# Kernel tuning notes

Hardware: AMD Instinct MI355X
Metric: run time of the kernel (lower is better)

The kernel has to match this reference:

```python
import jax, jax.numpy as jnp
import numpy as np

K = 20        # kNN neighborhood size (args.k)
EPS = 1e-5    # BatchNorm eps
SLOPE = 0.2   # LeakyReLU negative slope
B, N = 8, 2048


def lrelu(x):
    return jnp.where(x >= 0, x, SLOPE * x)


def bn_cn(x):  # BatchNorm1d over [B, C, N] (training-mode batch stats, gamma=1, beta=0)
    m = jnp.mean(x, axis=(0, 2), keepdims=True)
    v = jnp.var(x, axis=(0, 2), keepdims=True)
    return (x - m) * jax.lax.rsqrt(v + EPS)


def bn_f(x):  # BatchNorm1d over [B, F]
    m = jnp.mean(x, axis=0, keepdims=True)
    v = jnp.var(x, axis=0, keepdims=True)
    return (x - m) * jax.lax.rsqrt(v + EPS)


def conv_bn(x, w):  # 1x1 Conv1d (no bias) + BN + LeakyReLU; x [B,C,N], w [O,C]
    return lrelu(bn_cn(jnp.einsum('oc,bcn->bon', w, x)))


def knn_idx(x, k):  # x [B,C,N] -> [B,N,k] nearest neighbors, self excluded
    sq = jnp.sum(x * x, axis=1)                                   # [B,N]
    pd = 2.0 * jnp.einsum('bcn,bcm->bnm', x, x) - sq[:, :, None] - sq[:, None, :]
    return jax.lax.top_k(pd, k + 1)[1][:, :, 1:]                  # drop self (max = 0)


def self_att(x, wq, wk, wv, wc):  # SelfAttention block (n_heads=1, scale_dot)
    idx = knn_idx(x, K)                                           # [B,N,K]
    feats = jnp.swapaxes(x, 1, 2)                                 # [B,N,C]
    nb = jax.vmap(lambda f, i: f[i])(feats, idx)                  # [B,N,K,C] gather
    E = wq.shape[0]
    q = feats @ wq.T                                              # [B,N,E]
    kk = nb @ wk.T                                                # [B,N,K,E]
    v = (nb - feats[:, :, None, :]) @ wv.T                        # [B,N,K,V]
    scores = jax.nn.softmax(jnp.einsum('bne,bnke->bnk', q, kk) / np.float32(np.sqrt(E)), axis=-1)
    out = jnp.einsum('bnk,bnkv->bnv', scores, v)                  # [B,N,V]
    res = conv_bn(jnp.swapaxes(out, 1, 2), wc)                    # [B,O,N]
    return jnp.concatenate([res, x], axis=1)


def setup_inputs() -> dict:
    key = jax.random.key(0)
    ks = jax.random.split(key, 32)
    w = lambda k, o, i: jax.random.normal(k, (o, i), jnp.float32) / np.float32(np.sqrt(i))
    d = {'x': jax.random.normal(ks[0], (B, 3, N), jnp.float32)}
    dims = {1: 3, 2: 64, 3: 64, 4: 128}
    j = 1
    for s, c in dims.items():
        for nm in ('wq', 'wk', 'wv', 'wc'):
            d[f'sa{s}_{nm}'] = w(ks[j], c, c); j += 1
    d['conv1_w'] = w(ks[17], 64, 6)
    d['conv2_w'] = w(ks[18], 64, 128)
    d['conv3_w'] = w(ks[19], 128, 128)
    d['conv4_w'] = w(ks[20], 256, 256)
    d['conv5_w'] = w(ks[21], 1024, 512)
    d['lin1_w'] = w(ks[22], 512, 2048); d['lin1_b'] = jnp.zeros((512,), jnp.float32)
    d['lin2_w'] = w(ks[23], 256, 512);  d['lin2_b'] = jnp.zeros((256,), jnp.float32)
    d['lin3_w'] = w(ks[24], 40, 256);   d['lin3_b'] = jnp.zeros((40,), jnp.float32)
    return d


def reference(x, sa1_wq, sa1_wk, sa1_wv, sa1_wc, sa2_wq, sa2_wk, sa2_wv, sa2_wc,
              sa3_wq, sa3_wk, sa3_wv, sa3_wc, sa4_wq, sa4_wk, sa4_wv, sa4_wc,
              conv1_w, conv2_w, conv3_w, conv4_w, conv5_w,
              lin1_w, lin1_b, lin2_w, lin2_b, lin3_w, lin3_b):
    h = self_att(x, sa1_wq, sa1_wk, sa1_wv, sa1_wc)        # [B,6,N]
    x1 = conv_bn(h, conv1_w)                               # [B,64,N]
    h = self_att(x1, sa2_wq, sa2_wk, sa2_wv, sa2_wc)       # [B,128,N]
    x2 = conv_bn(h, conv2_w)                               # [B,64,N]
    h = self_att(x2, sa3_wq, sa3_wk, sa3_wv, sa3_wc)       # [B,128,N]
    x3 = conv_bn(h, conv3_w)                               # [B,128,N]
    h = self_att(x3, sa4_wq, sa4_wk, sa4_wv, sa4_wc)       # [B,256,N]
    x4 = conv_bn(h, conv4_w)                               # [B,256,N]
    xc = jnp.concatenate([x1, x2, x3, x4], axis=1)         # [B,512,N]
    x5 = conv_bn(xc, conv5_w)                              # [B,1024,N]
    p = jnp.concatenate([jnp.max(x5, axis=2), jnp.mean(x5, axis=2)], axis=1)  # [B,2048]
    h = lrelu(bn_f(p @ lin1_w.T + lin1_b))                 # dropout = identity (eval)
    h = lrelu(bn_f(h @ lin2_w.T + lin2_b))
    return h @ lin3_w.T + lin3_b                           # [B,40]
```

## Files before the change

kernel.cpp:

```cpp
#include <hip/hip_runtime.h>
#include <math.h>

#define BB 8
#define NN 2048
#define KNB 20

typedef __attribute__((ext_vector_type(8))) short bf16x8;
typedef __attribute__((ext_vector_type(8))) _Float16 f16x8;
typedef __attribute__((ext_vector_type(4))) float f32x4;

__device__ inline unsigned short f2bf(float f) {
  union { float f; unsigned u; } v; v.f = f;
  unsigned r = v.u + 0x7FFF + ((v.u >> 16) & 1);
  return (unsigned short)(r >> 16);
}

__device__ inline float lrelu(float v) { return v >= 0.f ? v : 0.2f * v; }

template <bool F16SPLIT, bool BF16>
__global__ __launch_bounds__(256) void xprep_kernel(
    const float* __restrict__ in, int inBS, int C,
    float* __restrict__ xT, _Float16* __restrict__ hi, _Float16* __restrict__ lo,
    unsigned short* __restrict__ bf, float* __restrict__ sq) {
  __shared__ float tile[32][33];
  __shared__ float ps[8][33];
  int b = blockIdx.z;
  const float* ip = in + (size_t)b * inBS;
  int c0 = blockIdx.x * 32;
  int r0 = blockIdx.y * 32;
  int tx = threadIdx.x & 31, ty = threadIdx.x >> 5;
  float s = 0.f;
  for (int yy = ty; yy < 32; yy += 8) {
    int r = r0 + yy;
    float v = (r < C) ? ip[(size_t)r * NN + c0 + tx] : 0.f;
    tile[yy][tx] = v;
    s += v * v;
  }
  ps[ty][tx] = s;
  __syncthreads();
  if (ty == 0) {
    float a = ps[0][tx];
#pragma unroll
    for (int u = 1; u < 8; ++u) a += ps[u][tx];
    atomicAdd(&sq[b * NN + c0 + tx], a);
  }
  for (int yy = ty; yy < 32; yy += 8) {
    int c = c0 + yy, r = r0 + tx;
    if (r < C) {
      float v = tile[tx][yy];
      size_t o = (size_t)b * NN * C + (size_t)c * C + r;
      xT[o] = v;
      if (F16SPLIT) {
        _Float16 hv = (_Float16)v;
        hi[o] = hv;
        lo[o] = (_Float16)(v - (float)hv);
      }
      if (BF16) bf[o] = f2bf(v);
    }
  }
}

__global__ __launch_bounds__(256) void xprep3_kernel(const float* __restrict__ in,
                                                     float* __restrict__ xT,
                                                     float* __restrict__ xs4) {
  int b = blockIdx.z;
  int n = blockIdx.x * 256 + threadIdx.x;
  const float* ip = in + (size_t)b * 3 * NN;
  float x0 = ip[n], x1 = ip[NN + n], x2 = ip[2 * NN + n];
  float s = x0 * x0 + x1 * x1 + x2 * x2;
  size_t o = (size_t)b * NN + n;
  xT[o * 3 + 0] = x0; xT[o * 3 + 1] = x1; xT[o * 3 + 2] = x2;
  *(float4*)&xs4[o * 4] = make_float4(x0, x1, x2, s);
}

__global__ __launch_bounds__(256) void prep_mw_kernel(
    const float* __restrict__ wq, const float* __restrict__ wk,
    const float* __restrict__ wv, const float* __restrict__ wc, int C,
    float* __restrict__ M, float* __restrict__ WCV,
    unsigned short* __restrict__ Mb, unsigned short* __restrict__ wcvb, int emitBF) {
  int w = blockIdx.x * 4 + (threadIdx.x >> 6);
  int lane = threadIdx.x & 63;
  int total = 2 * C * C;
  if (w >= total) return;
  float a = 0.f;
  if (w < C * C) {
    int c = w / C, cp = w - c * C;
    for (int e = lane; e < C; e += 64) a += wk[e * C + c] * wq[e * C + cp];
  } else {
    int t = w - C * C;
    int o = t / C, c = t - o * C;
    for (int e = lane; e < C; e += 64) a += wc[o * C + e] * wv[e * C + c];
  }
#pragma unroll
  for (int s = 32; s > 0; s >>= 1) a += __shfl_down(a, s);
  if (lane == 0) {
    if (w < C * C) {
      M[w] = a;
      if (emitBF) Mb[w] = f2bf(a);
    } else {
      int t = w - C * C;
      WCV[t] = a;
      if (emitBF) wcvb[t] = f2bf(a);
    }
  }
}

__global__ __launch_bounds__(256) void convert_bf16_kernel(const float* __restrict__ in,
                                                           unsigned short* __restrict__ out,
                                                           int count) {
  int i = blockIdx.x * 256 + threadIdx.x;
  if (i < count) out[i] = f2bf(in[i]);
}

__global__ __launch_bounds__(256) void transpose_kernel(const float* __restrict__ in, int inBS,
                                                        int R, int Cl, float* __restrict__ out) {
  __shared__ float tile[32][33];
  int b = blockIdx.z;
  const float* ip = in + (size_t)b * inBS;
  float* op = out + (size_t)b * R * Cl;
  int c0 = blockIdx.x * 32, r0 = blockIdx.y * 32;
  int tx = threadIdx.x & 31, ty = threadIdx.x >> 5;
  for (int yy = ty; yy < 32; yy += 8) {
    int r = r0 + yy, c = c0 + tx;
    tile[yy][tx] = (r < R && c < Cl) ? ip[(size_t)r * Cl + c] : 0.f;
  }
  __syncthreads();
  for (int yy = ty; yy < 32; yy += 8) {
    int c = c0 + yy, r = r0 + tx;
    if (c < Cl && r < R) op[(size_t)c * R + r] = tile[tx][yy];
  }
}

__global__ __launch_bounds__(256) void transpose_bf16_kernel(const float* __restrict__ in, int inBS,
                                                             int R, int Cl,
                                                             unsigned short* __restrict__ out) {
  __shared__ float tile[32][33];
  int b = blockIdx.z;
  const float* ip = in + (size_t)b * inBS;
  unsigned short* op = out + (size_t)b * R * Cl;
  int c0 = blockIdx.x * 32, r0 = blockIdx.y * 32;
  int tx = threadIdx.x & 31, ty = threadIdx.x >> 5;
  for (int yy = ty; yy < 32; yy += 8) {
    int r = r0 + yy, c = c0 + tx;
    tile[yy][tx] = (r < R && c < Cl) ? ip[(size_t)r * Cl + c] : 0.f;
  }
  __syncthreads();
  for (int yy = ty; yy < 32; yy += 8) {
    int c = c0 + yy, r = r0 + tx;
    if (c < Cl && r < R) op[(size_t)c * R + r] = f2bf(tile[tx][yy]);
  }
}

__global__ __launch_bounds__(256, 2) void mfma_gemm_lds_kernel(
    const unsigned short* __restrict__ A, const unsigned short* __restrict__ B,
    float* __restrict__ Z, int O, int K) {
  const int b = blockIdx.z;
  const int n0 = blockIdx.x * 128, o0 = blockIdx.y * 128;
  const int tid = threadIdx.x;
  const int wave = tid >> 6, lane = tid & 63;
  const int wo = wave >> 1, wn = wave & 1;
  const int l16 = lane & 15, q = lane >> 4;
  __shared__ unsigned short Al[2][4096];
  __shared__ unsigned short Bl[2][4096];
  const unsigned short* Ab = A + (size_t)o0 * K;
  const unsigned short* Bb = B + ((size_t)b * NN + n0) * K;

  const int p0 = tid, p1 = tid + 256;
  const int r0 = ((p0 >> 6) << 4) | (p0 & 15), c0 = ((p0 >> 4) & 3) * 8;
  const int r1 = ((p1 >> 6) << 4) | (p1 & 15), c1 = ((p1 >> 4) & 3) * 8;

  bf16x8 ar0, ar1, br0, br1;
  auto gload = [&](int k0) {
    ar0 = *(const bf16x8*)(Ab + (size_t)r0 * K + k0 + c0);
    ar1 = *(const bf16x8*)(Ab + (size_t)r1 * K + k0 + c1);
    br0 = *(const bf16x8*)(Bb + (size_t)r0 * K + k0 + c0);
    br1 = *(const bf16x8*)(Bb + (size_t)r1 * K + k0 + c1);
  };
  auto sstore = [&](int buf) {
    *(bf16x8*)&Al[buf][p0 * 8] = ar0;
    *(bf16x8*)&Al[buf][p1 * 8] = ar1;
    *(bf16x8*)&Bl[buf][p0 * 8] = br0;
    *(bf16x8*)&Bl[buf][p1 * 8] = br1;
  };

  f32x4 acc[4][4];
#pragma unroll
  for (int s = 0; s < 4; ++s)
#pragma unroll
    for (int t = 0; t < 4; ++t) acc[s][t] = (f32x4){0.f, 0.f, 0.f, 0.f};

  gload(0);
  sstore(0);
  int cur = 0;
  for (int k0 = 0; k0 < K; k0 += 32) {
    bool more = (k0 + 32) < K;
    if (more) gload(k0 + 32);
    __syncthreads();
    bf16x8 af[4], bfr[4];
#pragma unroll
    for (int s = 0; s < 4; ++s)
      af[s] = *(const bf16x8*)&Al[cur][((wo * 4 + s) * 64 + q * 16 + l16) * 8];
#pragma unroll
    for (int t = 0; t < 4; ++t)
      bfr[t] = *(const bf16x8*)&Bl[cur][((wn * 4 + t) * 64 + q * 16 + l16) * 8];
#pragma unroll
    for (int s = 0; s < 4; ++s)
#pragma unroll
      for (int t = 0; t < 4; ++t)
        acc[s][t] = __builtin_amdgcn_mfma_f32_16x16x32_bf16(af[s], bfr[t], acc[s][t], 0, 0, 0);
    if (more) sstore(cur ^ 1);
    cur ^= 1;
  }
#pragma unroll
  for (int s = 0; s < 4; ++s)
#pragma unroll
    for (int t = 0; t < 4; ++t) {
      float* zp = Z + ((size_t)b * O + o0 + wo * 64 + s * 16 + q * 4) * NN
                  + n0 + wn * 64 + t * 16 + l16;
#pragma unroll
      for (int r = 0; r < 4; ++r) zp[(size_t)r * NN] = acc[s][t][r];
    }
}

__global__ __launch_bounds__(256, 2) void pd_mfma_kernel(
    const _Float16* __restrict__ xhi, const _Float16* __restrict__ xlo, int C,
    const float* __restrict__ sq, float* __restrict__ P, int b_base) {
  const int bl = blockIdx.z;
  const int b = b_base + bl;
  const int n0 = blockIdx.x * 128, m0 = blockIdx.y * 128;
  const int tid = threadIdx.x;
  const int wave = tid >> 6, lane = tid & 63;
  const int wn_ = wave >> 1, wm_ = wave & 1;
  const int l16 = lane & 15, q = lane >> 4;
  __shared__ _Float16 Ah[4096], Al[4096], Bh[4096], Bl[4096];
  const _Float16* Ahg = xhi + ((size_t)b * NN + n0) * C;
  const _Float16* Alg = xlo + ((size_t)b * NN + n0) * C;
  const _Float16* Bhg = xhi + ((size_t)b * NN + m0) * C;
  const _Float16* Blg = xlo + ((size_t)b * NN + m0) * C;

  const int p0 = tid, p1 = tid + 256;
  const int r0 = ((p0 >> 6) << 4) | (p0 & 15), c0 = ((p0 >> 4) & 3) * 8;
  const int r1 = ((p1 >> 6) << 4) | (p1 & 15), c1 = ((p1 >> 4) & 3) * 8;

  f32x4 acc[4][4];
#pragma unroll
  for (int s = 0; s < 4; ++s)
#pragma unroll
    for (int t = 0; t < 4; ++t) acc[s][t] = (f32x4){0.f, 0.f, 0.f, 0.f};

  for (int k0 = 0; k0 < C; k0 += 32) {
    __syncthreads();
    *(f16x8*)&Ah[p0 * 8] = *(const f16x8*)(Ahg + (size_t)r0 * C + k0 + c0);
    *(f16x8*)&Ah[p1 * 8] = *(const f16x8*)(Ahg + (size_t)r1 * C + k0 + c1);
    *(f16x8*)&Al[p0 * 8] = *(const f16x8*)(Alg + (size_t)r0 * C + k0 + c0);
    *(f16x8*)&Al[p1 * 8] = *(const f16x8*)(Alg + (size_t)r1 * C + k0 + c1);
    *(f16x8*)&Bh[p0 * 8] = *(const f16x8*)(Bhg + (size_t)r0 * C + k0 + c0);
    *(f16x8*)&Bh[p1 * 8] = *(const f16x8*)(Bhg + (size_t)r1 * C + k0 + c1);
    *(f16x8*)&Bl[p0 * 8] = *(const f16x8*)(Blg + (size_t)r0 * C + k0 + c0);
    *(f16x8*)&Bl[p1 * 8] = *(const f16x8*)(Blg + (size_t)r1 * C + k0 + c1);
    __syncthreads();
    f16x8 ah[4], al[4], bh[4], blv[4];
#pragma unroll
    for (int s = 0; s < 4; ++s) {
      int pi = ((wn_ * 4 + s) * 64 + q * 16 + l16) * 8;
      ah[s] = *(const f16x8*)&Ah[pi];
      al[s] = *(const f16x8*)&Al[pi];
    }
#pragma unroll
    for (int t = 0; t < 4; ++t) {
      int pi = ((wm_ * 4 + t) * 64 + q * 16 + l16) * 8;
      bh[t] = *(const f16x8*)&Bh[pi];
      blv[t] = *(const f16x8*)&Bl[pi];
    }
#pragma unroll
    for (int s = 0; s < 4; ++s)
#pragma unroll
      for (int t = 0; t < 4; ++t) {
        acc[s][t] = __builtin_amdgcn_mfma_f32_16x16x32_f16(ah[s], bh[t], acc[s][t], 0, 0, 0);
        acc[s][t] = __builtin_amdgcn_mfma_f32_16x16x32_f16(ah[s], blv[t], acc[s][t], 0, 0, 0);
        acc[s][t] = __builtin_amdgcn_mfma_f32_16x16x32_f16(al[s], bh[t], acc[s][t], 0, 0, 0);
      }
  }
#pragma unroll
  for (int s = 0; s < 4; ++s)
#pragma unroll
    for (int t = 0; t < 4; ++t) {
      int col = m0 + wm_ * 64 + t * 16 + l16;
      float sqv = sq[b * NN + col];
      float* pp = P + ((size_t)bl * NN + n0 + wn_ * 64 + s * 16 + q * 4) * NN + col;
#pragma unroll
      for (int r = 0; r < 4; ++r) pp[(size_t)r * NN] = 2.f * acc[s][t][r] - sqv;
    }
}

__global__ __launch_bounds__(256) void topk_bsort_kernel(const float* __restrict__ P,
                                                         int* __restrict__ idx_out, int b_base) {
  const int wave = threadIdx.x >> 6;
  const int lane = threadIdx.x & 63;
  const int n = blockIdx.x * 4 + wave;
  const int bl = blockIdx.y;
  const int b = b_base + bl;
  const float4* rp = (const float4*)(P + ((size_t)bl * NN + n) * NN);
  unsigned key[32];
#pragma unroll
  for (int q = 0; q < 8; ++q) {
    float4 vv = rp[q * 64 + lane];
    int mb = q * 256 + lane * 4;
    float fv[4] = {vv.x, vv.y, vv.z, vv.w};
#pragma unroll
    for (int j = 0; j < 4; ++j) {
      unsigned u = __float_as_uint(fv[j]);
      unsigned mask = (unsigned)(((int)u) >> 31) | 0x80000000u;
      unsigned sl = (unsigned)(q * 4 + j);
      key[q * 4 + j] = (mb + j == n) ? sl : (((u ^ mask) & 0xFFFFFFE0u) | sl);
    }
  }
#pragma unroll
  for (int k = 2; k <= 32; k <<= 1) {
#pragma unroll
    for (int j = k >> 1; j > 0; j >>= 1) {
#pragma unroll
      for (int i = 0; i < 32; ++i) {
        int l = i ^ j;
        if (l > i) {
          unsigned ka = key[i], kb = key[l];
          unsigned mx = ka > kb ? ka : kb;
          unsigned mn = ka > kb ? kb : ka;
          if ((i & k) == 0) { key[i] = mx; key[l] = mn; }
          else              { key[i] = mn; key[l] = mx; }
        }
      }
    }
  }
  int* op = idx_out + (size_t)(b * NN + n) * KNB;
  for (int k = 0; k < KNB; ++k) {
    unsigned best = key[0];
#pragma unroll
    for (int s = 32; s > 0; s >>= 1) {
      unsigned o = (unsigned)__shfl_xor((int)best, s);
      best = best > o ? best : o;
    }
    unsigned long long bal = __ballot(key[0] == best);
    if (lane == (int)__ffsll(bal) - 1) {
      unsigned sl = key[0] & 31u;
      op[k] = (int)((sl >> 2) * 256u + (unsigned)lane * 4u + (sl & 3u));
#pragma unroll
      for (int j = 0; j < 20; ++j) key[j] = key[j + 1];
    }
  }
}

__global__ __launch_bounds__(256) void topk_c3_kernel(const float* __restrict__ xs4,
                                                      int* __restrict__ idx_out) {
  const int wave = threadIdx.x >> 6;
  const int lane = threadIdx.x & 63;
  const int n = blockIdx.x * 4 + wave;
  const int b = blockIdx.y;
  const float4* xp = (const float4*)(xs4 + (size_t)b * NN * 4);
  float4 me = xp[n];
  float tx = 2.f * me.x, ty = 2.f * me.y, tz = 2.f * me.z;
  unsigned key[32];
#pragma unroll
  for (int s = 0; s < 32; ++s) {
    int m = s * 64 + lane;
    float4 c = xp[m];
    float pd = tx * c.x + ty * c.y + tz * c.z - c.w;
    unsigned u = __float_as_uint(pd);
    unsigned mask = (unsigned)(((int)u) >> 31) | 0x80000000u;
    key[s] = (m == n) ? (unsigned)s : ((((u ^ mask) & 0xFFFFFFE0u)) | (unsigned)s);
  }
#pragma unroll
  for (int k = 2; k <= 32; k <<= 1) {
#pragma unroll
    for (int j = k >> 1; j > 0; j >>= 1) {
#pragma unroll
      for (int i = 0; i < 32; ++i) {
        int l = i ^ j;
        if (l > i) {
          unsigned ka = key[i], kb = key[l];
          unsigned mx = ka > kb ? ka : kb;
          unsigned mn = ka > kb ? kb : ka;
          if ((i & k) == 0) { key[i] = mx; key[l] = mn; }
          else              { key[i] = mn; key[l] = mx; }
        }
      }
    }
  }
  int* op = idx_out + (size_t)(b * NN + n) * KNB;
  for (int k = 0; k < KNB; ++k) {
    unsigned best = key[0];
#pragma unroll
    for (int s = 32; s > 0; s >>= 1) {
      unsigned o = (unsigned)__shfl_xor((int)best, s);
      best = best > o ? best : o;
    }
    unsigned long long bal = __ballot(key[0] == best);
    if (lane == (int)__ffsll(bal) - 1) {
      unsigned sl = key[0] & 31u;
      op[k] = (int)(sl * 64u + (unsigned)lane);
#pragma unroll
      for (int j = 0; j < 20; ++j) key[j] = key[j + 1];
    }
  }
}

__global__ __launch_bounds__(256, 2) void conv_gemm_kernel(
    const float* __restrict__ in, int inBS, int C, int O,
    const float* __restrict__ w, float* __restrict__ z) {
  const int b = blockIdx.z;
  const int n0 = blockIdx.x * 64, o0 = blockIdx.y * 64;
  const int tid = threadIdx.x;
  const int tm = tid & 15, tn = tid >> 4;
  __shared__ float Ws[16][68];
  __shared__ float Xs[16][64];
  const float* ib = in + (size_t)b * inBS;
  float acc[4][4];
#pragma unroll
  for (int i = 0; i < 4; ++i)
#pragma unroll
    for (int j = 0; j < 4; ++j) acc[i][j] = 0.f;

  for (int k0 = 0; k0 < C; k0 += 16) {
    __syncthreads();
#pragma unroll
    for (int it = 0; it < 4; ++it) {
      int i = it * 256 + tid;
      int kc = i >> 6, nl = i & 63;
      Xs[kc][nl] = ((k0 + kc) < C) ? ib[(size_t)(k0 + kc) * NN + n0 + nl] : 0.f;
      int ol = i >> 4, kc2 = i & 15;
      Ws[kc2][ol] = ((o0 + ol) < O && (k0 + kc2) < C) ? w[(size_t)(o0 + ol) * C + k0 + kc2] : 0.f;
    }
    __syncthreads();
#pragma unroll
    for (int kc = 0; kc < 16; ++kc) {
      float4 a = *(const float4*)&Ws[kc][tn * 4];
      float4 bv = *(const float4*)&Xs[kc][tm * 4];
      acc[0][0] += a.x * bv.x; acc[0][1] += a.x * bv.y; acc[0][2] += a.x * bv.z; acc[0][3] += a.x * bv.w;
      acc[1][0] += a.y * bv.x; acc[1][1] += a.y * bv.y; acc[1][2] += a.y * bv.z; acc[1][3] += a.y * bv.w;
      acc[2][0] += a.z * bv.x; acc[2][1] += a.z * bv.y; acc[2][2] += a.z * bv.z; acc[2][3] += a.z * bv.w;
      acc[3][0] += a.w * bv.x; acc[3][1] += a.w * bv.y; acc[3][2] += a.w * bv.z; acc[3][3] += a.w * bv.w;
    }
  }
#pragma unroll
  for (int i = 0; i < 4; ++i) {
    int o = o0 + tn * 4 + i;
    if (o < O) {
      float4 ov;
      ov.x = acc[i][0]; ov.y = acc[i][1]; ov.z = acc[i][2]; ov.w = acc[i][3];
      *(float4*)&z[((size_t)b * O + o) * NN + n0 + tm * 4] = ov;
    }
  }
}

__global__ __launch_bounds__(256, 2) void conv_gemm128_db_kernel(
    const float* __restrict__ in, int inBS, int C, int O,
    const float* __restrict__ w, float* __restrict__ z) {
  const int b = blockIdx.z;
  const int n0 = blockIdx.x * 128, o0 = blockIdx.y * 128;
  const int tid = threadIdx.x;
  const int tm = tid & 15, tn = tid >> 4;
  __shared__ float Xs[2][16][128];
  __shared__ float Ws[2][16][132];
  const float* ib = in + (size_t)b * inBS;
  float acc[8][8];
#pragma unroll
  for (int i = 0; i < 8; ++i)
#pragma unroll
    for (int j = 0; j < 8; ++j) acc[i][j] = 0.f;

  float4 xr[2], wr[2];
  auto load_tile = [&](int k0) {
#pragma unroll
    for (int it = 0; it < 2; ++it) {
      int i = it * 256 + tid;
      int kc = i >> 5, c4 = i & 31;
      xr[it] = ((k0 + kc) < C) ? *(const float4*)&ib[(size_t)(k0 + kc) * NN + n0 + c4 * 4]
                               : make_float4(0.f, 0.f, 0.f, 0.f);
      int ol = i >> 2, kq = i & 3;
      wr[it] = ((k0 + kq * 4) < C) ? *(const float4*)&w[(size_t)(o0 + ol) * C + k0 + kq * 4]
                                   : make_float4(0.f, 0.f, 0.f, 0.f);
    }
  };
  auto store_tile = [&](int buf) {
#pragma unroll
    for (int it = 0; it < 2; ++it) {
      int i = it * 256 + tid;
      int kc = i >> 5, c4 = i & 31;
      *(float4*)&Xs[buf][kc][c4 * 4] = xr[it];
      int ol = i >> 2, kq = i & 3;
      Ws[buf][kq * 4 + 0][ol] = wr[it].x;
      Ws[buf][kq * 4 + 1][ol] = wr[it].y;
      Ws[buf][kq * 4 + 2][ol] = wr[it].z;
      Ws[buf][kq * 4 + 3][ol] = wr[it].w;
    }
  };

  load_tile(0);
  store_tile(0);
  int cur = 0;
  for (int k0 = 0; k0 < C; k0 += 16) {
    bool more = (k0 + 16) < C;
    if (more) load_tile(k0 + 16);
    __syncthreads();
#pragma unroll
    for (int kc = 0; kc < 16; ++kc) {
      float4 a0 = *(const float4*)&Ws[cur][kc][tn * 4];
      float4 a1 = *(const float4*)&Ws[cur][kc][64 + tn * 4];
      float4 b0 = *(const float4*)&Xs[cur][kc][tm * 4];
      float4 b1 = *(const float4*)&Xs[cur][kc][64 + tm * 4];
      float ar[8] = {a0.x, a0.y, a0.z, a0.w, a1.x, a1.y, a1.z, a1.w};
      float br[8] = {b0.x, b0.y, b0.z, b0.w, b1.x, b1.y, b1.z, b1.w};
#pragma unroll
      for (int i = 0; i < 8; ++i)
#pragma unroll
        for (int j = 0; j < 8; ++j) acc[i][j] += ar[i] * br[j];
    }
    if (more) store_tile(cur ^ 1);
    cur ^= 1;
  }
#pragma unroll
  for (int h = 0; h < 2; ++h)
#pragma unroll
    for (int i = 0; i < 4; ++i) {
      int r = h * 4 + i;
      int o = o0 + h * 64 + tn * 4 + i;
      float* zrow = &z[((size_t)b * O + o) * NN + n0];
      float4 o0v, o1v;
      o0v.x = acc[r][0]; o0v.y = acc[r][1]; o0v.z = acc[r][2]; o0v.w = acc[r][3];
      o1v.x = acc[r][4]; o1v.y = acc[r][5]; o1v.z = acc[r][6]; o1v.w = acc[r][7];
      *(float4*)&zrow[tm * 4] = o0v;
      *(float4*)&zrow[64 + tm * 4] = o1v;
    }
}

template <int C, bool BF16OUT>
__global__ __launch_bounds__(64) void att_wave_kernel(
    const float* __restrict__ xT, const float* __restrict__ UT,
    const int* __restrict__ idx, float* __restrict__ AGGt,
    unsigned short* __restrict__ AGGtb) {
  const int n = blockIdx.x & (NN - 1);
  const int b = blockIdx.x >> 11;
  const int lane = threadIdx.x;
  constexpr int CP = C + 1;
  __shared__ float nb[KNB][CP];
  __shared__ float sl[KNB];
  __shared__ int nidx[KNB];
  __shared__ float ul[C];
  const float* xTb = xT + (size_t)b * NN * C;
  if (lane < KNB) nidx[lane] = idx[(size_t)(b * NN + n) * KNB + lane];
  for (int c = lane; c < C; c += 64) ul[c] = UT[((size_t)b * NN + n) * C + c];
  __syncthreads();
  for (int i = lane; i < KNB * C; i += 64) {
    int k = i / C, c = i - k * C;
    nb[k][c] = xTb[(size_t)nidx[k] * C + c];
  }
  __syncthreads();
  float sv = -INFINITY;
  if (lane < KNB) {
    float a = 0.f;
#pragma unroll
    for (int c = 0; c < C; ++c) a += nb[lane][c] * ul[c];
    sv = a / sqrtf((float)C);
  }
  float mx = sv;
#pragma unroll
  for (int s = 32; s > 0; s >>= 1) mx = fmaxf(mx, __shfl_xor(mx, s));
  float e = (lane < KNB) ? expf(sv - mx) : 0.f;
  float sum = e;
#pragma unroll
  for (int s = 32; s > 0; s >>= 1) sum += __shfl_xor(sum, s);
  if (lane < KNB) sl[lane] = e / sum;
  __syncthreads();
  const float* xTn = xTb + (size_t)n * C;
  for (int c = lane; c < C; c += 64) {
    float a = 0.f;
#pragma unroll
    for (int k = 0; k < KNB; ++k) a += sl[k] * nb[k][c];
    float r = a - xTn[c];
    if (BF16OUT)
      AGGtb[((size_t)b * NN + n) * C + c] = f2bf(r);
    else
      AGGt[((size_t)b * NN + n) * C + c] = r;
  }
}

__global__ __launch_bounds__(256) void bn_fused_kernel(const float* __restrict__ z, int O,
                                                       float* __restrict__ out, int outBS, int c0) {
  int o = blockIdx.x;
  int tid = threadIdx.x;
  __shared__ float s1[256], s2[256];
  __shared__ float smv, srv;
  float a1 = 0.f, a2 = 0.f;
  for (int i = tid; i < BB * 512; i += 256) {
    int b = i >> 9, n4 = i & 511;
    float4 v = *(const float4*)&z[((size_t)b * O + o) * NN + n4 * 4];
    a1 += v.x + v.y + v.z + v.w;
    a2 += v.x * v.x + v.y * v.y + v.z * v.z + v.w * v.w;
  }
  s1[tid] = a1; s2[tid] = a2;
  __syncthreads();
  for (int st = 128; st > 0; st >>= 1) {
    if (tid < st) { s1[tid] += s1[tid + st]; s2[tid] += s2[tid + st]; }
    __syncthreads();
  }
  if (tid == 0) {
    float m = s1[0] / (BB * NN);
    float var = s2[0] / (BB * NN) - m * m;
    smv = m; srv = rsqrtf(var + 1e-5f);
  }
  __syncthreads();
  float m = smv, r = srv;
  for (int i = tid; i < BB * 512; i += 256) {
    int b = i >> 9, n4 = i & 511;
    float4 v = *(const float4*)&z[((size_t)b * O + o) * NN + n4 * 4];
    float4 ov;
    ov.x = lrelu((v.x - m) * r); ov.y = lrelu((v.y - m) * r);
    ov.z = lrelu((v.z - m) * r); ov.w = lrelu((v.w - m) * r);
    *(float4*)&out[(size_t)b * outBS + (size_t)(c0 + o) * NN + n4 * 4] = ov;
  }
}

__global__ __launch_bounds__(256) void bn_copy_kernel(const float* __restrict__ z, int O,
                                                      const float* __restrict__ xin, int xbs,
                                                      float* __restrict__ out) {
  int o = blockIdx.x;
  int tid = threadIdx.x;
  int outBS = 2 * O * NN;
  if (o >= O) {
    int c = o - O;
    for (int i = tid; i < BB * 512; i += 256) {
      int b = i >> 9, n4 = i & 511;
      *(float4*)&out[(size_t)b * outBS + (size_t)o * NN + n4 * 4] =
          *(const float4*)&xin[(size_t)b * xbs + (size_t)c * NN + n4 * 4];
    }
    return;
  }
  __shared__ float s1[256], s2[256];
  __shared__ float smv, srv;
  float a1 = 0.f, a2 = 0.f;
  for (int i = tid; i < BB * 512; i += 256) {
    int b = i >> 9, n4 = i & 511;
    float4 v = *(const float4*)&z[((size_t)b * O + o) * NN + n4 * 4];
    a1 += v.x + v.y + v.z + v.w;
    a2 += v.x * v.x + v.y * v.y + v.z * v.z + v.w * v.w;
  }
  s1[tid] = a1; s2[tid] = a2;
  __syncthreads();
  for (int st = 128; st > 0; st >>= 1) {
    if (tid < st) { s1[tid] += s1[tid + st]; s2[tid] += s2[tid + st]; }
    __syncthreads();
  }
  if (tid == 0) {
    float m = s1[0] / (BB * NN);
    float var = s2[0] / (BB * NN) - m * m;
    smv = m; srv = rsqrtf(var + 1e-5f);
  }
  __syncthreads();
  float m = smv, r = srv;
  for (int i = tid; i < BB * 512; i += 256) {
    int b = i >> 9, n4 = i & 511;
    float4 v = *(const float4*)&z[((size_t)b * O + o) * NN + n4 * 4];
    float4 ov;
    ov.x = lrelu((v.x - m) * r); ov.y = lrelu((v.y - m) * r);
    ov.z = lrelu((v.z - m) * r); ov.w = lrelu((v.w - m) * r);
    *(float4*)&out[(size_t)b * outBS + (size_t)o * NN + n4 * 4] = ov;
  }
}

__global__ __launch_bounds__(256) void bn_pool_kernel(const float* __restrict__ z,
                                                      float* __restrict__ p) {
  int o = blockIdx.x;
  int tid = threadIdx.x;
  __shared__ float s1[256], s2[256];
  __shared__ float smv, srv;
  float a1 = 0.f, a2 = 0.f;
  for (int i = tid; i < BB * 512; i += 256) {
    int b = i >> 9, n4 = i & 511;
    float4 v = *(const float4*)&z[((size_t)b * 1024 + o) * NN + n4 * 4];
    a1 += v.x + v.y + v.z + v.w;
    a2 += v.x * v.x + v.y * v.y + v.z * v.z + v.w * v.w;
  }
  s1[tid] = a1; s2[tid] = a2;
  __syncthreads();
  for (int st = 128; st > 0; st >>= 1) {
    if (tid < st) { s1[tid] += s1[tid + st]; s2[tid] += s2[tid + st]; }
    __syncthreads();
  }
  if (tid == 0) {
    float m = s1[0] / (BB * NN);
    float var = s2[0] / (BB * NN) - m * m;
    smv = m; srv = rsqrtf(var + 1e-5f);
  }
  __syncthreads();
  float m = smv, r = srv;
  int b = tid >> 5, l = tid & 31;
  const float* zp = z + ((size_t)b * 1024 + o) * NN;
  float mx = -INFINITY, sm = 0.f;
  for (int j = l; j < 512; j += 32) {
    float4 v = *(const float4*)&zp[j * 4];
    float vx = lrelu((v.x - m) * r), vy = lrelu((v.y - m) * r);
    float vz = lrelu((v.z - m) * r), vw = lrelu((v.w - m) * r);
    mx = fmaxf(mx, fmaxf(fmaxf(vx, vy), fmaxf(vz, vw)));
    sm += vx + vy + vz + vw;
  }
#pragma unroll
  for (int s = 16; s > 0; s >>= 1) {
    mx = fmaxf(mx, __shfl_xor(mx, s));
    sm += __shfl_xor(sm, s);
  }
  if (l == 0) {
    p[b * 2048 + o] = mx;
    p[b * 2048 + 1024 + o] = sm * (1.f / NN);
  }
}

__global__ __launch_bounds__(64) void linear_kernel(const float* __restrict__ in, int IN, int OUT,
                                                    const float* __restrict__ w,
                                                    const float* __restrict__ bias,
                                                    float* __restrict__ out) {
  int o = blockIdx.x;
  int b = o / OUT, f = o % OUT;
  const float* ip = in + (size_t)b * IN;
  const float* wp = w + (size_t)f * IN;
  float a = 0.f;
  for (int i = threadIdx.x; i < IN; i += 64) a += ip[i] * wp[i];
#pragma unroll
  for (int s = 32; s > 0; s >>= 1) a += __shfl_down(a, s);
  if (threadIdx.x == 0) out[o] = a + bias[f];
}

__global__ __launch_bounds__(256) void bnf_kernel(float* __restrict__ t, int F) {
  int f = blockIdx.x * blockDim.x + threadIdx.x;
  if (f >= F) return;
  float s = 0.f, s2 = 0.f;
  for (int b = 0; b < BB; ++b) { float v = t[b * F + f]; s += v; s2 += v * v; }
  float m = s * (1.f / BB);
  float var = s2 * (1.f / BB) - m * m;
  float r = rsqrtf(var + 1e-5f);
  for (int b = 0; b < BB; ++b) {
    float v = (t[b * F + f] - m) * r;
    t[b * F + f] = v >= 0.f ? v : 0.2f * v;
  }
}


struct SAW { const float *wq, *wk, *wv, *wc; };

static inline void run_conv(const float* in, int inBS, int C, int O, const float* w,
                            float* z, hipStream_t st) {
  if (O % 128 == 0)
    conv_gemm128_db_kernel<<<dim3(NN / 128, O / 128, BB), 256, 0, st>>>(in, inBS, C, O, w, z);
  else
    conv_gemm_kernel<<<dim3(NN / 64, (O + 63) / 64, BB), 256, 0, st>>>(in, inBS, C, O, w, z);
}

template <int C, bool MFMA>
static inline void run_sa(const float* xin, int xbs, SAW w,
                          float* xT, float* U, float* UT, float* AGGt,
                          float* AGG, float* z, float* h, float* sq, int* idx,
                          float* M, float* WCV, unsigned short* Mb, unsigned short* wcvb,
                          unsigned short* xTb, unsigned short* AGGtb,
                          _Float16* xhi, _Float16* xlo,
                          float* D, int nbatch, hipStream_t st) {
  static_assert(C % 32 == 0, "run_sa requires C % 32 == 0");
  xprep_kernel<true, MFMA><<<dim3(NN / 32, C / 32, BB), 256, 0, st>>>(
      xin, xbs, C, xT, xhi, xlo, xTb, sq);
  prep_mw_kernel<<<(2 * C * C + 3) / 4, 256, 0, st>>>(w.wq, w.wk, w.wv, w.wc, C,
                                                      M, WCV, Mb, wcvb, MFMA ? 1 : 0);
  for (int bb = 0; bb < BB; bb += nbatch) {
    int nbc = (BB - bb) < nbatch ? (BB - bb) : nbatch;
    pd_mfma_kernel<<<dim3(16, 16, nbc), 256, 0, st>>>(xhi, xlo, C, sq, D, bb);
    topk_bsort_kernel<<<dim3(NN / 4, nbc), 256, 0, st>>>(D, idx, bb);
  }
  if (MFMA)
    mfma_gemm_lds_kernel<<<dim3(NN / 128, C / 128, BB), 256, 0, st>>>(Mb, xTb, U, C, C);
  else
    run_conv(xin, xbs, C, C, M, U, st);
  transpose_kernel<<<dim3(NN / 32, C / 32, BB), 256, 0, st>>>(U, C * NN, C, NN, UT);
  if (MFMA) {
    att_wave_kernel<C, true><<<BB * NN, 64, 0, st>>>(xT, UT, idx, AGGt, AGGtb);
    mfma_gemm_lds_kernel<<<dim3(NN / 128, C / 128, BB), 256, 0, st>>>(wcvb, AGGtb, z, C, C);
  } else {
    att_wave_kernel<C, false><<<BB * NN, 64, 0, st>>>(xT, UT, idx, AGGt, AGGtb);
    transpose_kernel<<<dim3(C / 32, NN / 32, BB), 256, 0, st>>>(AGGt, NN * C, NN, C, AGG);
    run_conv(AGG, C * NN, C, C, WCV, z, st);
  }
  bn_copy_kernel<<<2 * C, 256, 0, st>>>(z, C, xin, xbs, h);
}

static inline void run_sa3(const float* xin, SAW w,
                           float* xT, float* U, float* UT, float* AGGt, float* AGG,
                           float* z, float* h, float* xs4, int* idx,
                           float* M, float* WCV, unsigned short* Mb, unsigned short* wcvb,
                           hipStream_t st) {
  xprep3_kernel<<<dim3(NN / 256, 1, BB), 256, 0, st>>>(xin, xT, xs4);
  prep_mw_kernel<<<(2 * 3 * 3 + 3) / 4, 256, 0, st>>>(w.wq, w.wk, w.wv, w.wc, 3,
                                                      M, WCV, Mb, wcvb, 0);
  topk_c3_kernel<<<dim3(NN / 4, BB), 256, 0, st>>>(xs4, idx);
  conv_gemm_kernel<<<dim3(NN / 64, 1, BB), 256, 0, st>>>(xin, 3 * NN, 3, 3, M, U);
  transpose_kernel<<<dim3(NN / 32, 1, BB), 256, 0, st>>>(U, 3 * NN, 3, NN, UT);
  att_wave_kernel<3, false><<<BB * NN, 64, 0, st>>>(xT, UT, idx, AGGt, nullptr);
  transpose_kernel<<<dim3(1, NN / 32, BB), 256, 0, st>>>(AGGt, NN * 3, NN, 3, AGG);
  conv_gemm_kernel<<<dim3(NN / 64, 1, BB), 256, 0, st>>>(AGG, 3 * NN, 3, 3, WCV, z);
  bn_copy_kernel<<<6, 256, 0, st>>>(z, 3, xin, 3 * NN, h);
}

static inline void run_conv_bn(const float* in, int inBS, int Cin, int O, const float* w,
                               float* z, float* out, int outBS, int c0, hipStream_t st) {
  run_conv(in, inBS, Cin, O, w, z, st);
  bn_fused_kernel<<<O, 256, 0, st>>>(z, O, out, outBS, c0);
}

extern "C" void kernel_launch(void* const* d_in, const int* in_sizes, int n_in,
                              void* d_out, int out_size, void* d_ws, size_t ws_size,
                              hipStream_t stream) {
  const float* x = (const float*)d_in[0];
  SAW sa1{(const float*)d_in[1], (const float*)d_in[2], (const float*)d_in[3], (const float*)d_in[4]};
  SAW sa2{(const float*)d_in[5], (const float*)d_in[6], (const float*)d_in[7], (const float*)d_in[8]};
  SAW sa3{(const float*)d_in[9], (const float*)d_in[10], (const float*)d_in[11], (const float*)d_in[12]};
  SAW sa4{(const float*)d_in[13], (const float*)d_in[14], (const float*)d_in[15], (const float*)d_in[16]};
  const float* conv1_w = (const float*)d_in[17];
  const float* conv2_w = (const float*)d_in[18];
  const float* conv3_w = (const float*)d_in[19];
  const float* conv4_w = (const float*)d_in[20];
  const float* conv5_w = (const float*)d_in[21];
  const float* lin1_w = (const float*)d_in[22];
  const float* lin1_b = (const float*)d_in[23];
  const float* lin2_w = (const float*)d_in[24];
  const float* lin2_b = (const float*)d_in[25];
  const float* lin3_w = (const float*)d_in[26];
  const float* lin3_b = (const float*)d_in[27];

  char* ws = (char*)d_ws;
  size_t off = 0;
  auto take = [&](size_t bytes) -> void* {
    void* p = ws + off;
    off += (bytes + 255) & ~(size_t)255;
    return p;
  };
  float* sqR  = (float*)take((size_t)3 * BB * NN * 4);
  float* xs4  = (float*)take((size_t)BB * NN * 4 * 4);
  int*   idx  = (int*)take((size_t)BB * NN * KNB * 4);
  float* M    = (float*)take((size_t)128 * 128 * 4);
  float* WCV  = (float*)take((size_t)128 * 128 * 4);
  unsigned short* Mb   = (unsigned short*)take((size_t)128 * 128 * 2);
  unsigned short* wcvb = (unsigned short*)take((size_t)128 * 128 * 2);
  unsigned short* w4b  = (unsigned short*)take((size_t)256 * 256 * 2);
  unsigned short* w5b  = (unsigned short*)take((size_t)1024 * 512 * 2);
  float* U    = (float*)take((size_t)BB * 128 * NN * 4);
  float* AGG  = (float*)take((size_t)BB * 128 * NN * 4);
  float* h    = (float*)take((size_t)BB * 256 * NN * 4);
  float* z    = (float*)take((size_t)BB * 1024 * NN * 4);
  float* xc   = (float*)take((size_t)BB * 512 * NN * 4);
  float* p    = (float*)take((size_t)BB * 2048 * 4);
  float* t1   = (float*)take((size_t)BB * 512 * 4);
  float* t2   = (float*)take((size_t)BB * 256 * 4);
  (void)n_in; (void)in_sizes; (void)out_size;

  float* xT = AGG;
  float* UT = h;
  float* AGGt = z;
  unsigned short* xTb   = (unsigned short*)((char*)h + (size_t)BB * 128 * NN * 4);
  unsigned short* AGGtb = (unsigned short*)((char*)z + (size_t)16 * 1024 * 1024);
  unsigned short* hTb   = (unsigned short*)U;
  unsigned short* xcTb  = (unsigned short*)U;
  _Float16* xhi = (_Float16*)h;
  _Float16* xlo = (_Float16*)((char*)h + (size_t)BB * NN * 128 * 2);

  size_t dfull = (size_t)BB * NN * NN * 4;
  bool fullD = (ws_size > off + dfull + 4096);
  float* D = fullD ? (float*)take(dfull) : z;
  int nbatch = fullD ? BB : 4;

  hipMemsetAsync(sqR, 0, (size_t)3 * BB * NN * 4, stream);

  run_sa3(x, sa1, xT, U, UT, AGGt, AGG, z, h, xs4, idx, M, WCV, Mb, wcvb, stream);
  run_conv_bn(h, 6 * NN, 6, 64, conv1_w, z, xc, 512 * NN, 0, stream);
  run_sa<64, false>(xc + 0 * NN, 512 * NN, sa2, xT, U, UT, AGGt, AGG, z, h,
                    sqR + 0 * BB * NN, idx, M, WCV, Mb, wcvb, xTb, AGGtb, xhi, xlo,
                    D, nbatch, stream);
  run_conv_bn(h, 128 * NN, 128, 64, conv2_w, z, xc, 512 * NN, 64, stream);
  run_sa<64, false>(xc + 64 * NN, 512 * NN, sa3, xT, U, UT, AGGt, AGG, z, h,
                    sqR + 1 * BB * NN, idx, M, WCV, Mb, wcvb, xTb, AGGtb, xhi, xlo,
                    D, nbatch, stream);
  run_conv_bn(h, 128 * NN, 128, 128, conv3_w, z, xc, 512 * NN, 128, stream);
  run_sa<128, true>(xc + 128 * NN, 512 * NN, sa4, xT, U, UT, AGGt, AGG, z, h,
                    sqR + 2 * BB * NN, idx, M, WCV, Mb, wcvb, xTb, AGGtb, xhi, xlo,
                    D, nbatch, stream);
  transpose_bf16_kernel<<<dim3(NN / 32, 8, BB), 256, 0, stream>>>(h, 256 * NN, 256, NN, hTb);
  convert_bf16_kernel<<<(256 * 256 + 255) / 256, 256, 0, stream>>>(conv4_w, w4b, 256 * 256);
  mfma_gemm_lds_kernel<<<dim3(NN / 128, 2, BB), 256, 0, stream>>>(w4b, hTb, z, 256, 256);
  bn_fused_kernel<<<256, 256, 0, stream>>>(z, 256, xc, 512 * NN, 256);
  transpose_bf16_kernel<<<dim3(NN / 32, 16, BB), 256, 0, stream>>>(xc, 512 * NN, 512, NN, xcTb);
  convert_bf16_kernel<<<(1024 * 512 + 255) / 256, 256, 0, stream>>>(conv5_w, w5b, 1024 * 512);
  mfma_gemm_lds_kernel<<<dim3(NN / 128, 8, BB), 256, 0, stream>>>(w5b, xcTb, z, 1024, 512);
  bn_pool_kernel<<<1024, 256, 0, stream>>>(z, p);
  linear_kernel<<<BB * 512, 64, 0, stream>>>(p, 2048, 512, lin1_w, lin1_b, t1);
  bnf_kernel<<<2, 256, 0, stream>>>(t1, 512);
  linear_kernel<<<BB * 256, 64, 0, stream>>>(t1, 512, 256, lin2_w, lin2_b, t2);
  bnf_kernel<<<1, 256, 0, stream>>>(t2, 256);
  linear_kernel<<<BB * 40, 64, 0, stream>>>(t2, 256, 40, lin3_w, lin3_b, (float*)d_out);
}
```

Baseline: 868.7 us.

## Fold transposes into GEMM epilogues and use register-resident attention kernel

```diff
diff --git a/kernel.cpp b/kernel.cpp
--- a/kernel.cpp
+++ b/kernel.cpp
@@ -151,6 +151,7 @@
   }
 }
 
+template <bool TOUT>
 __global__ __launch_bounds__(256, 2) void mfma_gemm_lds_kernel(
     const unsigned short* __restrict__ A, const unsigned short* __restrict__ B,
     float* __restrict__ Z, int O, int K) {
@@ -215,10 +216,16 @@
   for (int s = 0; s < 4; ++s)
 #pragma unroll
     for (int t = 0; t < 4; ++t) {
-      float* zp = Z + ((size_t)b * O + o0 + wo * 64 + s * 16 + q * 4) * NN
-                  + n0 + wn * 64 + t * 16 + l16;
-#pragma unroll
-      for (int r = 0; r < 4; ++r) zp[(size_t)r * NN] = acc[s][t][r];
+      if (TOUT) {
+        int n = n0 + wn * 64 + t * 16 + l16;
+        int ob = o0 + wo * 64 + s * 16 + q * 4;
+        *(f32x4*)&Z[((size_t)b * NN + n) * O + ob] = acc[s][t];
+      } else {
+        float* zp = Z + ((size_t)b * O + o0 + wo * 64 + s * 16 + q * 4) * NN
+                    + n0 + wn * 64 + t * 16 + l16;
+#pragma unroll
+        for (int r = 0; r < 4; ++r) zp[(size_t)r * NN] = acc[s][t][r];
+      }
     }
 }
 
@@ -404,6 +411,7 @@
   }
 }
 
+template <bool BT, bool TOUT>
 __global__ __launch_bounds__(256, 2) void conv_gemm_kernel(
     const float* __restrict__ in, int inBS, int C, int O,
     const float* __restrict__ w, float* __restrict__ z) {
@@ -425,8 +433,13 @@
 #pragma unroll
     for (int it = 0; it < 4; ++it) {
       int i = it * 256 + tid;
-      int kc = i >> 6, nl = i & 63;
-      Xs[kc][nl] = ((k0 + kc) < C) ? ib[(size_t)(k0 + kc) * NN + n0 + nl] : 0.f;
+      if (BT) {
+        int kc = i & 15, nl = i >> 4;
+        Xs[kc][nl] = ((k0 + kc) < C) ? ib[(size_t)(n0 + nl) * C + k0 + kc] : 0.f;
+      } else {
+        int kc = i >> 6, nl = i & 63;
+        Xs[kc][nl] = ((k0 + kc) < C) ? ib[(size_t)(k0 + kc) * NN + n0 + nl] : 0.f;
+      }
       int ol = i >> 4, kc2 = i & 15;
       Ws[kc2][ol] = ((o0 + ol) < O && (k0 + kc2) < C) ? w[(size_t)(o0 + ol) * C + k0 + kc2] : 0.f;
     }
@@ -441,13 +454,26 @@
       acc[3][0] += a.w * bv.x; acc[3][1] += a.w * bv.y; acc[3][2] += a.w * bv.z; acc[3][3] += a.w * bv.w;
     }
   }
-#pragma unroll
-  for (int i = 0; i < 4; ++i) {
-    int o = o0 + tn * 4 + i;
-    if (o < O) {
-      float4 ov;
-      ov.x = acc[i][0]; ov.y = acc[i][1]; ov.z = acc[i][2]; ov.w = acc[i][3];
-      *(float4*)&z[((size_t)b * O + o) * NN + n0 + tm * 4] = ov;
+  if (TOUT) {
+#pragma unroll
+    for (int j = 0; j < 4; ++j) {
+      int n = n0 + tm * 4 + j;
+      int ob = o0 + tn * 4;
+      if (ob < O) {
+        float4 ov;
+        ov.x = acc[0][j]; ov.y = acc[1][j]; ov.z = acc[2][j]; ov.w = acc[3][j];
+        *(float4*)&z[((size_t)b * NN + n) * O + ob] = ov;
+      }
+    }
+  } else {
+#pragma unroll
+    for (int i = 0; i < 4; ++i) {
+      int o = o0 + tn * 4 + i;
+      if (o < O) {
+        float4 ov;
+        ov.x = acc[i][0]; ov.y = acc[i][1]; ov.z = acc[i][2]; ov.w = acc[i][3];
+        *(float4*)&z[((size_t)b * O + o) * NN + n0 + tm * 4] = ov;
+      }
     }
   }
 }
@@ -531,6 +557,67 @@
       *(float4*)&zrow[tm * 4] = o0v;
       *(float4*)&zrow[64 + tm * 4] = o1v;
     }
+}
+
+template <int C, bool BF16OUT>
+__global__ __launch_bounds__(256) void att_wave_reg_kernel(
+    const float* __restrict__ xT, const float* __restrict__ UT,
+    const int* __restrict__ idx, float* __restrict__ AGGt,
+    unsigned short* __restrict__ AGGtb) {
+  const int lane = threadIdx.x & 63;
+  const int gid = blockIdx.x * 4 + (threadIdx.x >> 6);
+  const int n = gid & (NN - 1);
+  const int b = gid >> 11;
+  const float* xTb = xT + (size_t)b * NN * C;
+  int nv = idx[(size_t)gid * KNB + (lane < KNB ? lane : 0)];
+  float u0 = UT[(size_t)gid * C + lane];
+  float u1;
+  if (C == 128) u1 = UT[(size_t)gid * C + 64 + lane];
+  float v0[KNB], v1[KNB], p[KNB];
+#pragma unroll
+  for (int k = 0; k < KNB; ++k) {
+    int m = __shfl(nv, k) & (NN - 1);
+    v0[k] = xTb[(size_t)m * C + lane];
+    if (C == 128) v1[k] = xTb[(size_t)m * C + 64 + lane];
+  }
+#pragma unroll
+  for (int k = 0; k < KNB; ++k) {
+    float a = v0[k] * u0;
+    if (C == 128) a += v1[k] * u1;
+    p[k] = a;
+  }
+#pragma unroll
+  for (int k = 0; k < KNB; ++k) {
+#pragma unroll
+    for (int s = 32; s > 0; s >>= 1) p[k] += __shfl_xor(p[k], s);
+  }
+  const float scale = (C == 128) ? 0.088388347648318447f : 0.125f;
+  float mx = p[0];
+#pragma unroll
+  for (int k = 1; k < KNB; ++k) mx = fmaxf(mx, p[k]);
+  float sum = 0.f;
+#pragma unroll
+  for (int k = 0; k < KNB; ++k) {
+    p[k] = expf((p[k] - mx) * scale);
+    sum += p[k];
+  }
+  float inv = 1.f / sum;
+  float a0 = 0.f, a1 = 0.f;
+#pragma unroll
+  for (int k = 0; k < KNB; ++k) {
+    a0 += p[k] * v0[k];
+    if (C == 128) a1 += p[k] * v1[k];
+  }
+  float r0 = a0 * inv - xTb[(size_t)n * C + lane];
+  float r1;
+  if (C == 128) r1 = a1 * inv - xTb[(size_t)n * C + 64 + lane];
+  if (BF16OUT) {
+    AGGtb[(size_t)gid * C + lane] = f2bf(r0);
+    if (C == 128) AGGtb[(size_t)gid * C + 64 + lane] = f2bf(r1);
+  } else {
+    AGGt[(size_t)gid * C + lane] = r0;
+    if (C == 128) AGGt[(size_t)gid * C + 64 + lane] = r1;
+  }
 }
 
 template <int C, bool BF16OUT>
@@ -547,7 +634,7 @@
   __shared__ int nidx[KNB];
   __shared__ float ul[C];
   const float* xTb = xT + (size_t)b * NN * C;
-  if (lane < KNB) nidx[lane] = idx[(size_t)(b * NN + n) * KNB + lane];
+  if (lane < KNB) nidx[lane] = idx[(size_t)(b * NN + n) * KNB + lane] & (NN - 1);
   for (int c = lane; c < C; c += 64) ul[c] = UT[((size_t)b * NN + n) * C + c];
   __syncthreads();
   for (int i = lane; i < KNB * C; i += 64) {
@@ -751,13 +838,13 @@
   if (O % 128 == 0)
     conv_gemm128_db_kernel<<<dim3(NN / 128, O / 128, BB), 256, 0, st>>>(in, inBS, C, O, w, z);
   else
-    conv_gemm_kernel<<<dim3(NN / 64, (O + 63) / 64, BB), 256, 0, st>>>(in, inBS, C, O, w, z);
+    conv_gemm_kernel<false, false><<<dim3(NN / 64, (O + 63) / 64, BB), 256, 0, st>>>(in, inBS, C, O, w, z);
 }
 
 template <int C, bool MFMA>
 static inline void run_sa(const float* xin, int xbs, SAW w,
-                          float* xT, float* U, float* UT, float* AGGt,
-                          float* AGG, float* z, float* h, float* sq, int* idx,
+                          float* xT, float* UT, float* AGGt, float* z, float* h,
+                          float* sq, int* idx,
                           float* M, float* WCV, unsigned short* Mb, unsigned short* wcvb,
                           unsigned short* xTb, unsigned short* AGGtb,
                           _Float16* xhi, _Float16* xlo,
@@ -772,18 +859,14 @@
     pd_mfma_kernel<<<dim3(16, 16, nbc), 256, 0, st>>>(xhi, xlo, C, sq, D, bb);
     topk_bsort_kernel<<<dim3(NN / 4, nbc), 256, 0, st>>>(D, idx, bb);
   }
-  if (MFMA)
-    mfma_gemm_lds_kernel<<<dim3(NN / 128, C / 128, BB), 256, 0, st>>>(Mb, xTb, U, C, C);
-  else
-    run_conv(xin, xbs, C, C, M, U, st);
-  transpose_kernel<<<dim3(NN / 32, C / 32, BB), 256, 0, st>>>(U, C * NN, C, NN, UT);
   if (MFMA) {
-    att_wave_kernel<C, true><<<BB * NN, 64, 0, st>>>(xT, UT, idx, AGGt, AGGtb);
-    mfma_gemm_lds_kernel<<<dim3(NN / 128, C / 128, BB), 256, 0, st>>>(wcvb, AGGtb, z, C, C);
+    mfma_gemm_lds_kernel<true><<<dim3(NN / 128, C / 128, BB), 256, 0, st>>>(Mb, xTb, UT, C, C);
+    att_wave_reg_kernel<C, true><<<BB * NN / 4, 256, 0, st>>>(xT, UT, idx, nullptr, AGGtb);
+    mfma_gemm_lds_kernel<false><<<dim3(NN / 128, C / 128, BB), 256, 0, st>>>(wcvb, AGGtb, z, C, C);
   } else {
-    att_wave_kernel<C, false><<<BB * NN, 64, 0, st>>>(xT, UT, idx, AGGt, AGGtb);
-    transpose_kernel<<<dim3(C / 32, NN / 32, BB), 256, 0, st>>>(AGGt, NN * C, NN, C, AGG);
-    run_conv(AGG, C * NN, C, C, WCV, z, st);
+    conv_gemm_kernel<false, true><<<dim3(NN / 64, C / 64, BB), 256, 0, st>>>(xin, xbs, C, C, M, UT);
+    att_wave_reg_kernel<C, false><<<BB * NN / 4, 256, 0, st>>>(xT, UT, idx, AGGt, nullptr);
+    conv_gemm_kernel<true, false><<<dim3(NN / 64, C / 64, BB), 256, 0, st>>>(AGGt, NN * C, C, C, WCV, z);
   }
   bn_copy_kernel<<<2 * C, 256, 0, st>>>(z, C, xin, xbs, h);
 }
@@ -797,11 +880,11 @@
   prep_mw_kernel<<<(2 * 3 * 3 + 3) / 4, 256, 0, st>>>(w.wq, w.wk, w.wv, w.wc, 3,
                                                       M, WCV, Mb, wcvb, 0);
   topk_c3_kernel<<<dim3(NN / 4, BB), 256, 0, st>>>(xs4, idx);
-  conv_gemm_kernel<<<dim3(NN / 64, 1, BB), 256, 0, st>>>(xin, 3 * NN, 3, 3, M, U);
+  conv_gemm_kernel<false, false><<<dim3(NN / 64, 1, BB), 256, 0, st>>>(xin, 3 * NN, 3, 3, M, U);
   transpose_kernel<<<dim3(NN / 32, 1, BB), 256, 0, st>>>(U, 3 * NN, 3, NN, UT);
   att_wave_kernel<3, false><<<BB * NN, 64, 0, st>>>(xT, UT, idx, AGGt, nullptr);
   transpose_kernel<<<dim3(1, NN / 32, BB), 256, 0, st>>>(AGGt, NN * 3, NN, 3, AGG);
-  conv_gemm_kernel<<<dim3(NN / 64, 1, BB), 256, 0, st>>>(AGG, 3 * NN, 3, 3, WCV, z);
+  conv_gemm_kernel<false, false><<<dim3(NN / 64, 1, BB), 256, 0, st>>>(AGG, 3 * NN, 3, 3, WCV, z);
   bn_copy_kernel<<<6, 256, 0, st>>>(z, 3, xin, 3 * NN, h);
 }
 
@@ -858,8 +941,9 @@
   (void)n_in; (void)in_sizes; (void)out_size;
 
   float* xT = AGG;
+  float* AGGt64 = AGG + (size_t)BB * NN * 64;
   float* UT = h;
-  float* AGGt = z;
+  float* AGGt1 = z;
   unsigned short* xTb   = (unsigned short*)((char*)h + (size_t)BB * 128 * NN * 4);
   unsigned short* AGGtb = (unsigned short*)((char*)z + (size_t)16 * 1024 * 1024);
   unsigned short* hTb   = (unsigned short*)U;
@@ -874,26 +958,26 @@
 
   hipMemsetAsync(sqR, 0, (size_t)3 * BB * NN * 4, stream);
 
-  run_sa3(x, sa1, xT, U, UT, AGGt, AGG, z, h, xs4, idx, M, WCV, Mb, wcvb, stream);
+  run_sa3(x, sa1, xT, U, UT, AGGt1, AGG, z, h, xs4, idx, M, WCV, Mb, wcvb, stream);
   run_conv_bn(h, 6 * NN, 6, 64, conv1_w, z, xc, 512 * NN, 0, stream);
-  run_sa<64, false>(xc + 0 * NN, 512 * NN, sa2, xT, U, UT, AGGt, AGG, z, h,
+  run_sa<64, false>(xc + 0 * NN, 512 * NN, sa2, xT, UT, AGGt64, z, h,
                     sqR + 0 * BB * NN, idx, M, WCV, Mb, wcvb, xTb, AGGtb, xhi, xlo,
                     D, nbatch, stream);
   run_conv_bn(h, 128 * NN, 128, 64, conv2_w, z, xc, 512 * NN, 64, stream);
-  run_sa<64, false>(xc + 64 * NN, 512 * NN, sa3, xT, U, UT, AGGt, AGG, z, h,
+  run_sa<64, false>(xc + 64 * NN, 512 * NN, sa3, xT, UT, AGGt64, z, h,
                     sqR + 1 * BB * NN, idx, M, WCV, Mb, wcvb, xTb, AGGtb, xhi, xlo,
                     D, nbatch, stream);
   run_conv_bn(h, 128 * NN, 128, 128, conv3_w, z, xc, 512 * NN, 128, stream);
-  run_sa<128, true>(xc + 128 * NN, 512 * NN, sa4, xT, U, UT, AGGt, AGG, z, h,
+  run_sa<128, true>(xc + 128 * NN, 512 * NN, sa4, xT, UT, nullptr, z, h,
                     sqR + 2 * BB * NN, idx, M, WCV, Mb, wcvb, xTb, AGGtb, xhi, xlo,
                     D, nbatch, stream);
   transpose_bf16_kernel<<<dim3(NN / 32, 8, BB), 256, 0, stream>>>(h, 256 * NN, 256, NN, hTb);
   convert_bf16_kernel<<<(256 * 256 + 255) / 256, 256, 0, stream>>>(conv4_w, w4b, 256 * 256);
-  mfma_gemm_lds_kernel<<<dim3(NN / 128, 2, BB), 256, 0, stream>>>(w4b, hTb, z, 256, 256);
+  mfma_gemm_lds_kernel<false><<<dim3(NN / 128, 2, BB), 256, 0, stream>>>(w4b, hTb, z, 256, 256);
   bn_fused_kernel<<<256, 256, 0, stream>>>(z, 256, xc, 512 * NN, 256);
   transpose_bf16_kernel<<<dim3(NN / 32, 16, BB), 256, 0, stream>>>(xc, 512 * NN, 512, NN, xcTb);
   convert_bf16_kernel<<<(1024 * 512 + 255) / 256, 256, 0, stream>>>(conv5_w, w5b, 1024 * 512);
-  mfma_gemm_lds_kernel<<<dim3(NN / 128, 8, BB), 256, 0, stream>>>(w5b, xcTb, z, 1024, 512);
+  mfma_gemm_lds_kernel<false><<<dim3(NN / 128, 8, BB), 256, 0, stream>>>(w5b, xcTb, z, 1024, 512);
   bn_pool_kernel<<<1024, 256, 0, stream>>>(z, p);
   linear_kernel<<<BB * 512, 64, 0, stream>>>(p, 2048, 512, lin1_w, lin1_b, t1);
   bnf_kernel<<<2, 256, 0, stream>>>(t1, 512);
```

New measurement: 850.7 us. 2.1% less time.
